# Performance work log

Measured on AMD Instinct MI355X. Metric: run time of the kernel, lower is better.

## Reference

```python
import jax
import jax.numpy as jnp
import numpy as np

TIME_DIVISION = 2
FILL_DIST = 50000.0  # sentinel initial distance, as in the torch module


def setup_inputs() -> dict:
    key = jax.random.key(0)
    k1, k2 = jax.random.split(key)
    B, T, H, W, C = 4, 16, 28, 28, 35
    TT = T // TIME_DIVISION
    x = jax.random.normal(k1, (B, T, H, W, C), dtype=jnp.float32)
    init_ = jax.random.randint(k2, (B * TIME_DIVISION,), 0, TT * H * W, dtype=jnp.int64)
    return {"x": x, "init_": init_, "k": 256}


def _pairwise_dist(xf):
    # xf: (Bt, N, C) -> (Bt, N, N) euclidean distances (torch.cdist p=2)
    sq = jnp.sum(xf * xf, axis=-1)                      # (Bt, N)
    gram = jnp.einsum('bnc,bmc->bnm', xf, xf)           # (Bt, N, N)
    d2 = jnp.maximum(sq[:, :, None] + sq[:, None, :] - 2.0 * gram, 0.0)
    return jnp.sqrt(d2)


def reference(x, init_, k):
    B, T, H, W, C = x.shape
    TT = T // TIME_DIVISION
    N = TT * H * W                 # points per time segment
    Bt = B * TIME_DIVISION
    k_ = k // TIME_DIVISION

    xf = x.reshape(Bt, N, C)
    cdist = _pairwise_dist(xf)
    # set diagonal to -1 (self-distance excluded from argmax)
    diag = jnp.arange(N)
    cdist = cdist.at[:, diag, diag].set(-1.0)

    b_idx = jnp.arange(Bt)
    farthest0 = jnp.remainder(init_, N)
    distance0 = jnp.full((Bt, N), FILL_DIST, dtype=x.dtype)

    def step(carry, _):
        distance, farthest = carry
        dist = cdist[b_idx, farthest]                   # (Bt, N) gather rows
        distance = jnp.minimum(dist, distance)
        farthest = jnp.argmax(distance, axis=-1)
        return (distance, farthest), farthest

    _, rest = jax.lax.scan(step, (distance0, farthest0), None, length=k_ - 1)
    sampling_index = jnp.concatenate([farthest0[None], rest], axis=0).T  # (Bt, k_)

    # add per-time-segment index offsets, flatten to (B, td*k_)
    offsets = (jnp.arange(TIME_DIVISION) * (TT * H * W))[None, :, None]
    sampling_index = sampling_index.reshape(B, TIME_DIVISION, k_) + offsets
    sampling_index = sampling_index.reshape(B, TIME_DIVISION * k_)

    # gather feature channels (first C-3; last 3 are positional encodings)
    xflat = x.reshape(B, T * H * W, C)
    patches = xflat[jnp.arange(B)[:, None], sampling_index][:, :, : C - 3]
    return patches, sampling_index
```

## Files before the change

### kernel.cpp

```cpp
#include <hip/hip_runtime.h>


#define NPTS 6272
#define CDIM 35
#define BT   8
#define KSEL 128
#define THW  12544
#define BPS  16
#define PPB  392
#define BLK  256
#define NB   (BT * BPS)
#define TAILN (PPB - BLK)

__device__ __forceinline__ unsigned long long key_of(float v, int j) {
  unsigned int u = __float_as_uint(v);
  u = (u & 0x80000000u) ? ~u : (u | 0x80000000u);
  return ((unsigned long long)u << 32) | (unsigned int)(NPTS - j);
}
__device__ __forceinline__ unsigned long long kmax(unsigned long long a,
                                                   unsigned long long b) {
  return a > b ? a : b;
}

__global__ __attribute__((amdgpu_waves_per_eu(1, 1))) __launch_bounds__(BLK)
void fps_kernel(const float* __restrict__ x,
                const int* __restrict__ init_,
                int* __restrict__ out_idx,
                unsigned long long* __restrict__ slots) {
  __shared__ unsigned long long wk[4];
  __shared__ int far_s;

  const int bid  = (int)blockIdx.x;
  const int b    = bid / BPS;
  const int sub  = bid % BPS;
  const int tid  = (int)threadIdx.x;
  const int lane = tid & 63;
  const int wid  = tid >> 6;
  const int j0   = sub * PPB;
  const float* xg = x + (size_t)b * NPTS * CDIM;
  unsigned long long* seg = slots + (size_t)b * KSEL * BPS;

  float xr0[CDIM], xr1[CDIM];
  float sqr0, sqr1, df0, df1;
  {
    const float* src0 = xg + (size_t)(j0 + tid) * CDIM;
    float acc = 0.0f;
    {
#pragma clang fp contract(off)
#pragma unroll
      for (int c = 0; c < CDIM; ++c) { float v = src0[c]; xr0[c] = v; acc = acc + v * v; }
    }
    sqr0 = acc; df0 = 50000.0f;
    sqr1 = 0.0f; df1 = 50000.0f;
#pragma unroll
    for (int c = 0; c < CDIM; ++c) xr1[c] = 0.0f;
    if (tid < TAILN) {
      const float* src1 = xg + (size_t)(j0 + BLK + tid) * CDIM;
      float acc1 = 0.0f;
      {
#pragma clang fp contract(off)
#pragma unroll
        for (int c = 0; c < CDIM; ++c) { float v = src1[c]; xr1[c] = v; acc1 = acc1 + v * v; }
      }
      sqr1 = acc1;
    }
#pragma unroll
    for (int c = 0; c < CDIM; ++c) {
      asm volatile("" : "+v"(xr0[c]));
      asm volatile("" : "+v"(xr1[c]));
    }
    asm volatile("" : "+v"(sqr0));
    asm volatile("" : "+v"(sqr1));
  }

  int far;
  { int f = init_[b] % NPTS; if (f < 0) f += NPTS; far = f; }
  if (sub == 0 && tid == 0) out_idx[b * KSEL] = far;

  for (int step = 1; step < KSEL; ++step) {
    const int fu = __builtin_amdgcn_readfirstlane(far);
    const float* fx = xg + (size_t)fu * CDIM;
    float xf[CDIM];
#pragma unroll
    for (int c = 0; c < CDIM; ++c) xf[c] = fx[c];

    float sqf;
    {
#pragma clang fp contract(off)
      float a = 0.0f;
#pragma unroll
      for (int c = 0; c < CDIM; ++c) { float t = xf[c]; a = a + t * t; }
      sqf = a;
    }

    unsigned long long bk;
    {
      float dot = 0.0f;
#pragma unroll
      for (int c = 0; c < CDIM; ++c)
        dot = __builtin_fmaf(xf[c], xr0[c], dot);
      float d2;
      {
#pragma clang fp contract(off)
        d2 = (sqf + sqr0) - 2.0f * dot;
      }
      d2 = fmaxf(d2, 0.0f);
      float d = __fsqrt_rn(d2);
      const int j = j0 + tid;
      d = (j == far) ? -1.0f : d;
      float nd = fminf(d, df0);
      df0 = nd;
      bk = key_of(nd, j);
    }
    if (tid < TAILN) {
      float dot = 0.0f;
#pragma unroll
      for (int c = 0; c < CDIM; ++c)
        dot = __builtin_fmaf(xf[c], xr1[c], dot);
      float d2;
      {
#pragma clang fp contract(off)
        d2 = (sqf + sqr1) - 2.0f * dot;
      }
      d2 = fmaxf(d2, 0.0f);
      float d = __fsqrt_rn(d2);
      const int j = j0 + BLK + tid;
      d = (j == far) ? -1.0f : d;
      float nd = fminf(d, df1);
      df1 = nd;
      bk = kmax(bk, key_of(nd, j));
    }

#pragma unroll
    for (int off = 32; off > 0; off >>= 1)
      bk = kmax(bk, __shfl_down(bk, off));
    if (lane == 0) wk[wid] = bk;
    __syncthreads();

    if (tid < BPS) {
      if (tid == 0) {
        unsigned long long m = kmax(kmax(wk[0], wk[1]), kmax(wk[2], wk[3]));
        __hip_atomic_store(&seg[step * BPS + sub], m,
                           __ATOMIC_RELAXED, __HIP_MEMORY_SCOPE_AGENT);
      }
      asm volatile("" ::: "memory");
      unsigned long long k;
      do {
        k = __hip_atomic_load(&seg[step * BPS + tid],
                              __ATOMIC_RELAXED, __HIP_MEMORY_SCOPE_AGENT);
      } while (k == 0ull);
#pragma unroll
      for (int off = 8; off > 0; off >>= 1)
        k = kmax(k, __shfl_down(k, off));
      if (tid == 0) {
        int f = NPTS - (int)(unsigned int)(k & 0xFFFFFFFFull);
        far_s = f;
        if (sub == 0) out_idx[b * KSEL + step] = f;
      }
    }
    __syncthreads();
    far = far_s;
  }
}

__global__ __launch_bounds__(256) void gather_kernel(const float* __restrict__ x,
                                                     const int* __restrict__ out_idx,
                                                     float* __restrict__ patches,
                                                     float* __restrict__ sidx) {
  const int b = (int)blockIdx.x;
  const int m = (int)threadIdx.x;
  const int td = m >> 7;
  const int i  = m & 127;
  const int li = out_idx[(b * 2 + td) * KSEL + i];
  const int gi = li + td * NPTS;
  sidx[b * 256 + m] = (float)gi;
  const float* src = x + ((size_t)b * THW + gi) * CDIM;
  float* dst = patches + ((size_t)b * 256 + m) * 32;
#pragma unroll
  for (int c = 0; c < 32; ++c) dst[c] = src[c];
}

extern "C" void kernel_launch(void* const* d_in, const int* in_sizes, int n_in,
                              void* d_out, int out_size, void* d_ws, size_t ws_size,
                              hipStream_t stream) {
  const float* x    = (const float*)d_in[0];
  const int*   init = (const int*)d_in[1];
  (void)in_sizes; (void)n_in; (void)out_size; (void)ws_size;

  unsigned long long* slots = (unsigned long long*)d_ws;
  const size_t slots_bytes = (size_t)BT * KSEL * BPS * sizeof(unsigned long long);
  int* idx = (int*)((char*)d_ws + slots_bytes);

  float* patches = (float*)d_out;
  float* sidx    = patches + (size_t)4 * 256 * 32;

  hipMemsetAsync(d_ws, 0, slots_bytes, stream);

  void* kargs[] = { (void*)&x, (void*)&init, (void*)&idx, (void*)&slots };
  hipLaunchCooperativeKernel((const void*)fps_kernel, dim3(NB), dim3(BLK),
                             kargs, 0, stream);

  hipLaunchKernelGGL(gather_kernel, dim3(4), dim3(256), 0, stream,
                     x, idx, patches, sidx);
}
```

Measured before the change: 270.7 us.

## Add XCD-local fast mailbox alongside device-scope slots for cross-block argmax exchange

Inter-block argmax exchange now writes each partial key to two mailboxes. One is a store with sc0 cache bits that lets readers on the same XCD see it through the shared L2. The other is the existing agent-scope atomic. Pollers read both with inline asm and take whichever is nonzero. The block-to-batch mapping becomes bid&7, presumably so all blocks of a batch share an XCD under round-robin dispatch. This aims to cut the per-step synchronization latency, but it relies on undocumented cache-coherence behaviour and dispatch order.

```diff
diff --git a/kernel.cpp b/kernel.cpp
--- a/kernel.cpp
+++ b/kernel.cpp
@@ -22,23 +22,45 @@
   return a > b ? a : b;
 }
 
+__device__ __forceinline__ void dual_store(unsigned long long* fp,
+                                           unsigned long long* sp,
+                                           unsigned long long v) {
+  asm volatile("global_store_dwordx2 %0, %1, off sc0"
+               :: "v"(fp), "v"(v) : "memory");
+  __hip_atomic_store(sp, v, __ATOMIC_RELAXED, __HIP_MEMORY_SCOPE_AGENT);
+}
+
+__device__ __forceinline__ void dual_load(const unsigned long long* fp,
+                                          const unsigned long long* sp,
+                                          unsigned long long& kf,
+                                          unsigned long long& ks) {
+  asm volatile("global_load_dwordx2 %0, %2, off sc0\n\t"
+               "global_load_dwordx2 %1, %3, off sc0 sc1\n\t"
+               "s_waitcnt vmcnt(0)"
+               : "=&v"(kf), "=&v"(ks)
+               : "v"(fp), "v"(sp)
+               : "memory");
+}
+
 __global__ __attribute__((amdgpu_waves_per_eu(1, 1))) __launch_bounds__(BLK)
 void fps_kernel(const float* __restrict__ x,
                 const int* __restrict__ init_,
                 int* __restrict__ out_idx,
-                unsigned long long* __restrict__ slots) {
+                unsigned long long* __restrict__ slow_slots,
+                unsigned long long* __restrict__ fast_slots) {
   __shared__ unsigned long long wk[4];
   __shared__ int far_s;
 
   const int bid  = (int)blockIdx.x;
-  const int b    = bid / BPS;
-  const int sub  = bid % BPS;
+  const int b    = bid & 7;
+  const int sub  = bid >> 3;
   const int tid  = (int)threadIdx.x;
   const int lane = tid & 63;
   const int wid  = tid >> 6;
   const int j0   = sub * PPB;
   const float* xg = x + (size_t)b * NPTS * CDIM;
-  unsigned long long* seg = slots + (size_t)b * KSEL * BPS;
+  unsigned long long* sseg = slow_slots + (size_t)b * KSEL * BPS;
+  unsigned long long* fseg = fast_slots + (size_t)b * KSEL * BPS;
 
   float xr0[CDIM], xr1[CDIM];
   float sqr0, sqr1, df0, df1;
@@ -140,14 +162,16 @@
     if (tid < BPS) {
       if (tid == 0) {
         unsigned long long m = kmax(kmax(wk[0], wk[1]), kmax(wk[2], wk[3]));
-        __hip_atomic_store(&seg[step * BPS + sub], m,
-                           __ATOMIC_RELAXED, __HIP_MEMORY_SCOPE_AGENT);
+        dual_store(&fseg[step * BPS + sub], &sseg[step * BPS + sub], m);
       }
       asm volatile("" ::: "memory");
-      unsigned long long k;
+      unsigned long long k = 0ull;
+      const unsigned long long* fp = &fseg[step * BPS + tid];
+      const unsigned long long* sp = &sseg[step * BPS + tid];
       do {
-        k = __hip_atomic_load(&seg[step * BPS + tid],
-                              __ATOMIC_RELAXED, __HIP_MEMORY_SCOPE_AGENT);
+        unsigned long long kf, ks;
+        dual_load(fp, sp, kf, ks);
+        k = ks ? ks : kf;
       } while (k == 0ull);
 #pragma unroll
       for (int off = 8; off > 0; off >>= 1)
@@ -187,16 +211,18 @@
   const int*   init = (const int*)d_in[1];
   (void)in_sizes; (void)n_in; (void)out_size; (void)ws_size;
 
-  unsigned long long* slots = (unsigned long long*)d_ws;
-  const size_t slots_bytes = (size_t)BT * KSEL * BPS * sizeof(unsigned long long);
-  int* idx = (int*)((char*)d_ws + slots_bytes);
+  const size_t arr = (size_t)BT * KSEL * BPS * sizeof(unsigned long long);
+  unsigned long long* slow_slots = (unsigned long long*)d_ws;
+  unsigned long long* fast_slots = (unsigned long long*)((char*)d_ws + arr);
+  int* idx = (int*)((char*)d_ws + 2 * arr);
 
   float* patches = (float*)d_out;
   float* sidx    = patches + (size_t)4 * 256 * 32;
 
-  hipMemsetAsync(d_ws, 0, slots_bytes, stream);
-
-  void* kargs[] = { (void*)&x, (void*)&init, (void*)&idx, (void*)&slots };
+  hipMemsetAsync(d_ws, 0, 2 * arr, stream);
+
+  void* kargs[] = { (void*)&x, (void*)&init, (void*)&idx,
+                    (void*)&slow_slots, (void*)&fast_slots };
   hipLaunchCooperativeKernel((const void*)fps_kernel, dim3(NB), dim3(BLK),
                              kargs, 0, stream);
 
```

Result: faster. 243.7 us (-10.0%).

## Use DPP wave reductions, pipelined inline-asm polling, and interleaved block-to-batch mapping

Applied to the files above, without the earlier changes.

Replaces the shuffle-based 64-lane and 16-lane max reductions with DPP row and broadcast operations plus readlane. The cross-block slot polling becomes hand-written assembly that keeps three pending split 32-bit loads in flight, so the ready flag is checked more often. Block-to-batch assignment is interleaved (b = bid & 7) so the blocks of one batch spread across more CUs or XCDs. The polling asm reads each 64-bit slot as two separate dwords, which risks a torn read, and it relies on specific cache-coherence bits (sc0 sc1).

```diff
diff --git a/kernel.cpp b/kernel.cpp
--- a/kernel.cpp
+++ b/kernel.cpp
@@ -22,6 +22,82 @@
   return a > b ? a : b;
 }
 
+template <int CTRL, int RMASK, bool BC>
+__device__ __forceinline__ unsigned long long dpp_kmax(unsigned long long k) {
+  unsigned int lo = (unsigned int)k, hi = (unsigned int)(k >> 32);
+  unsigned int tlo = (unsigned int)__builtin_amdgcn_update_dpp(0, (int)lo, CTRL, RMASK, 0xF, BC);
+  unsigned int thi = (unsigned int)__builtin_amdgcn_update_dpp(0, (int)hi, CTRL, RMASK, 0xF, BC);
+  unsigned long long t = ((unsigned long long)thi << 32) | tlo;
+  return kmax(k, t);
+}
+
+__device__ __forceinline__ unsigned long long wave_kmax64(unsigned long long k) {
+  k = dpp_kmax<0x111, 0xF, true >(k);
+  k = dpp_kmax<0x112, 0xF, true >(k);
+  k = dpp_kmax<0x114, 0xF, true >(k);
+  k = dpp_kmax<0x118, 0xF, true >(k);
+  k = dpp_kmax<0x142, 0xA, false>(k);
+  k = dpp_kmax<0x143, 0xC, false>(k);
+  unsigned int rlo = (unsigned int)__builtin_amdgcn_readlane((int)(unsigned int)k, 63);
+  unsigned int rhi = (unsigned int)__builtin_amdgcn_readlane((int)(k >> 32), 63);
+  return ((unsigned long long)rhi << 32) | rlo;
+}
+
+__device__ __forceinline__ unsigned long long row16_kmax(unsigned long long k) {
+  k = dpp_kmax<0x111, 0xF, true>(k);
+  k = dpp_kmax<0x112, 0xF, true>(k);
+  k = dpp_kmax<0x114, 0xF, true>(k);
+  k = dpp_kmax<0x118, 0xF, true>(k);
+  unsigned int rlo = (unsigned int)__builtin_amdgcn_readlane((int)(unsigned int)k, 15);
+  unsigned int rhi = (unsigned int)__builtin_amdgcn_readlane((int)(k >> 32), 15);
+  return ((unsigned long long)rhi << 32) | rlo;
+}
+
+__device__ __forceinline__ unsigned long long poll_slot(const unsigned long long* p) {
+  unsigned int klo = 0u, khi = 0u;
+  unsigned int a0, b0, a1, b1, a2, b2, t;
+  asm volatile(
+      "global_load_dword %[a0], %[ad], off sc0 sc1\n\t"
+      "global_load_dword %[b0], %[ad], off offset:4 sc0 sc1\n\t"
+      "global_load_dword %[a1], %[ad], off sc0 sc1\n\t"
+      "global_load_dword %[b1], %[ad], off offset:4 sc0 sc1\n\t"
+      "global_load_dword %[a2], %[ad], off sc0 sc1\n\t"
+      "global_load_dword %[b2], %[ad], off offset:4 sc0 sc1\n\t"
+      "1:\n\t"
+      "s_waitcnt vmcnt(4)\n\t"
+      "v_max_u32 %[klo], %[klo], %[a0]\n\t"
+      "v_max_u32 %[khi], %[khi], %[b0]\n\t"
+      "global_load_dword %[a0], %[ad], off sc0 sc1\n\t"
+      "global_load_dword %[b0], %[ad], off offset:4 sc0 sc1\n\t"
+      "v_min_u32 %[t], %[klo], %[khi]\n\t"
+      "v_cmp_eq_u32 vcc, 0, %[t]\n\t"
+      "s_cbranch_vccz 9f\n\t"
+      "s_waitcnt vmcnt(4)\n\t"
+      "v_max_u32 %[klo], %[klo], %[a1]\n\t"
+      "v_max_u32 %[khi], %[khi], %[b1]\n\t"
+      "global_load_dword %[a1], %[ad], off sc0 sc1\n\t"
+      "global_load_dword %[b1], %[ad], off offset:4 sc0 sc1\n\t"
+      "v_min_u32 %[t], %[klo], %[khi]\n\t"
+      "v_cmp_eq_u32 vcc, 0, %[t]\n\t"
+      "s_cbranch_vccz 9f\n\t"
+      "s_waitcnt vmcnt(4)\n\t"
+      "v_max_u32 %[klo], %[klo], %[a2]\n\t"
+      "v_max_u32 %[khi], %[khi], %[b2]\n\t"
+      "global_load_dword %[a2], %[ad], off sc0 sc1\n\t"
+      "global_load_dword %[b2], %[ad], off offset:4 sc0 sc1\n\t"
+      "v_min_u32 %[t], %[klo], %[khi]\n\t"
+      "v_cmp_eq_u32 vcc, 0, %[t]\n\t"
+      "s_cbranch_vccnz 1b\n\t"
+      "9:\n\t"
+      "s_waitcnt vmcnt(0)"
+      : [klo] "+v"(klo), [khi] "+v"(khi),
+        [a0] "=&v"(a0), [b0] "=&v"(b0), [a1] "=&v"(a1), [b1] "=&v"(b1),
+        [a2] "=&v"(a2), [b2] "=&v"(b2), [t] "=&v"(t)
+      : [ad] "v"(p)
+      : "vcc", "memory");
+  return ((unsigned long long)khi << 32) | klo;
+}
+
 __global__ __attribute__((amdgpu_waves_per_eu(1, 1))) __launch_bounds__(BLK)
 void fps_kernel(const float* __restrict__ x,
                 const int* __restrict__ init_,
@@ -31,8 +107,8 @@
   __shared__ int far_s;
 
   const int bid  = (int)blockIdx.x;
-  const int b    = bid / BPS;
-  const int sub  = bid % BPS;
+  const int b    = bid & 7;
+  const int sub  = bid >> 3;
   const int tid  = (int)threadIdx.x;
   const int lane = tid & 63;
   const int wid  = tid >> 6;
@@ -131,9 +207,7 @@
       bk = kmax(bk, key_of(nd, j));
     }
 
-#pragma unroll
-    for (int off = 32; off > 0; off >>= 1)
-      bk = kmax(bk, __shfl_down(bk, off));
+    bk = wave_kmax64(bk);
     if (lane == 0) wk[wid] = bk;
     __syncthreads();
 
@@ -144,14 +218,8 @@
                            __ATOMIC_RELAXED, __HIP_MEMORY_SCOPE_AGENT);
       }
       asm volatile("" ::: "memory");
-      unsigned long long k;
-      do {
-        k = __hip_atomic_load(&seg[step * BPS + tid],
-                              __ATOMIC_RELAXED, __HIP_MEMORY_SCOPE_AGENT);
-      } while (k == 0ull);
-#pragma unroll
-      for (int off = 8; off > 0; off >>= 1)
-        k = kmax(k, __shfl_down(k, off));
+      unsigned long long k = poll_slot(&seg[step * BPS + tid]);
+      k = row16_kmax(k);
       if (tid == 0) {
         int f = NPTS - (int)(unsigned int)(k & 0xFFFFFFFFull);
         far_s = f;
```

Result: faster. 225.3 us (-16.8%).
